# Optimization experiments

Measured on AMD Instinct MI355X. Metric: run time of the kernel, lower is better.

## Reference

```python
import jax, jax.numpy as jnp
import numpy as np

B, T, C, H = 4, 4096, 1024, 64

def setup_inputs() -> dict:
    key = jax.random.key(0)
    kx, kk, kq, kv = jax.random.split(key, 4)
    x = jax.random.normal(kx, (B, T, C), dtype=jnp.float32)
    Wk = jax.random.normal(kk, (C, H), dtype=jnp.float32) * (C ** -0.5)
    Wq = jax.random.normal(kq, (C, H), dtype=jnp.float32) * (C ** -0.5)
    Wv = jax.random.normal(kv, (C, H), dtype=jnp.float32) * (C ** -0.5)
    return {"x": x, "Wk": Wk, "Wq": Wq, "Wv": Wv}

def reference(x, Wk, Wq, Wv):
    Bb, Tt, Cc = x.shape
    k = jnp.einsum('btc,ch->bth', x, Wk)
    q = jnp.einsum('btc,ch->bth', x, Wq)
    v = jnp.einsum('btc,ch->bth', x, Wv)
    # NOTE: source scales by C**-0.5 with C = embed dim (not head_size)
    scores = jnp.einsum('bqh,bkh->bqk', q, k) * (Cc ** -0.5)
    causal = jnp.tril(jnp.ones((Tt, Tt), dtype=bool))
    scores = jnp.where(causal, scores, -jnp.inf)
    weights = jax.nn.softmax(scores, axis=-1)
    out = jnp.einsum('bqk,bkh->bqh', weights, v)
    return out
```

## Files before the change

kernel.cpp:

```cpp
#include <hip/hip_runtime.h>
#include <hip/hip_bf16.h>

typedef _Float16 f16x8 __attribute__((ext_vector_type(8)));
typedef _Float16 f16x4 __attribute__((ext_vector_type(4)));
typedef __fp16 fp16x2 __attribute__((ext_vector_type(2)));
typedef float f32x4 __attribute__((ext_vector_type(4)));

#define BATCH 4
#define SEQ 4096
#define EMB 1024
#define HEAD 64

__device__ __forceinline__ void async_copy16(const void* gsrc, void* ldst) {
  __builtin_amdgcn_global_load_lds(
      (const __attribute__((address_space(1))) void*)gsrc,
      (__attribute__((address_space(3))) void*)ldst,
      16, 0, 0);
}

__global__ __launch_bounds__(256) void wtrans_kernel(
    const float* __restrict__ Wk, const float* __restrict__ Wq,
    const float* __restrict__ Wv, _Float16* __restrict__ WT) {
  int id = blockIdx.x * 256 + threadIdx.x;
  int step = id / 1536;
  int rem = id - step * 1536;
  int G = rem / 192;
  int n = rem - G * 192;
  int sel = n >> 6;
  int col = n & 63;
  const float* src = (sel == 0) ? Wq : (sel == 1) ? Wk : Wv;
  const float scale = (sel == 0) ? 0.03125f : 1.0f;
  f16x8 u;
#pragma unroll
  for (int j = 0; j < 8; ++j) {
    int k = step * 64 + G * 8 + j;
    u[j] = (_Float16)(src[k * 64 + col] * scale);
  }
  *(f16x8*)(WT + (size_t)id * 8) = u;
}

__global__ __launch_bounds__(256) void proj_kernel(
    const float* __restrict__ x, const _Float16* __restrict__ WT,
    _Float16* __restrict__ Qh, _Float16* __restrict__ KT,
    _Float16* __restrict__ VT) {
  __shared__ _Float16 wtl[2][12288];
  __shared__ float xls[2][32 * 64];
  const int tid = threadIdx.x;
  const int wave = tid >> 6;
  const int lane = tid & 63;
  const int quad = lane >> 4;
  const int l16 = lane & 15;
  const int wm = wave & 1;
  const int wn = wave >> 1;
  const int rowblk = blockIdx.x * 32;

  const int lq = lane >> 4;
  const int pos = lane & 15;

  f32x4 acc[6];
#pragma unroll
  for (int t = 0; t < 6; ++t) acc[t] = (f32x4){0.f, 0.f, 0.f, 0.f};

#pragma unroll
  for (int i = 0; i < 6; ++i) {
    const int c = wave * 6 + i;
    async_copy16(WT + (size_t)c * 512 + lane * 8, (char*)&wtl[0][0] + c * 1024);
  }
#pragma unroll
  for (int i = 0; i < 2; ++i) {
    const int c = wave * 2 + i;
    const int rt = c * 4 + lq;
    const int u = pos ^ (rt & 7);
    async_copy16(x + (size_t)(rowblk + rt) * EMB + u * 4,
                 (char*)&xls[0][0] + c * 1024);
  }
  __syncthreads();

  const int rt = wm * 16 + l16;
  const int rb = rt & 7;
  const int ua = ((quad * 2) ^ rb) * 4;
  const int ub = ((quad * 2 + 1) ^ rb) * 4;
  const int uc = ((8 + quad * 2) ^ rb) * 4;
  const int ud = ((8 + quad * 2 + 1) ^ rb) * 4;

  int p = 0;
  for (int step = 0; step < 16; ++step) {
    if (step < 15) {
      const _Float16* wsrc = WT + (size_t)(step + 1) * 12288;
#pragma unroll
      for (int i = 0; i < 6; ++i) {
        const int c = wave * 6 + i;
        async_copy16(wsrc + (size_t)c * 512 + lane * 8,
                     (char*)&wtl[p ^ 1][0] + c * 1024);
      }
      const float* xsrc = x + (size_t)(step + 1) * 64;
#pragma unroll
      for (int i = 0; i < 2; ++i) {
        const int c = wave * 2 + i;
        const int rts = c * 4 + lq;
        const int u = pos ^ (rts & 7);
        async_copy16(xsrc + (size_t)(rowblk + rts) * EMB + u * 4,
                     (char*)&xls[p ^ 1][0] + c * 1024);
      }
    }
    const float* xl = &xls[p][rt * 64];
    const float4 xa = *(const float4*)(xl + ua);
    const float4 xb = *(const float4*)(xl + ub);
    const float4 xc = *(const float4*)(xl + uc);
    const float4 xd = *(const float4*)(xl + ud);
    fp16x2 p0 = __builtin_amdgcn_cvt_pkrtz(xa.x, xa.y);
    fp16x2 p1 = __builtin_amdgcn_cvt_pkrtz(xa.z, xa.w);
    fp16x2 p2 = __builtin_amdgcn_cvt_pkrtz(xb.x, xb.y);
    fp16x2 p3 = __builtin_amdgcn_cvt_pkrtz(xb.z, xb.w);
    f16x8 af0, af1;
    af0[0] = (_Float16)p0[0]; af0[1] = (_Float16)p0[1];
    af0[2] = (_Float16)p1[0]; af0[3] = (_Float16)p1[1];
    af0[4] = (_Float16)p2[0]; af0[5] = (_Float16)p2[1];
    af0[6] = (_Float16)p3[0]; af0[7] = (_Float16)p3[1];
    p0 = __builtin_amdgcn_cvt_pkrtz(xc.x, xc.y);
    p1 = __builtin_amdgcn_cvt_pkrtz(xc.z, xc.w);
    p2 = __builtin_amdgcn_cvt_pkrtz(xd.x, xd.y);
    p3 = __builtin_amdgcn_cvt_pkrtz(xd.z, xd.w);
    af1[0] = (_Float16)p0[0]; af1[1] = (_Float16)p0[1];
    af1[2] = (_Float16)p1[0]; af1[3] = (_Float16)p1[1];
    af1[4] = (_Float16)p2[0]; af1[5] = (_Float16)p2[1];
    af1[6] = (_Float16)p3[0]; af1[7] = (_Float16)p3[1];
#pragma unroll
    for (int t = 0; t < 6; ++t) {
      const int n = wn * 96 + t * 16 + l16;
      const f16x8 b0 = *(const f16x8*)&wtl[p][(size_t)((0 * 4 + quad) * 192 + n) * 8];
      const f16x8 b1 = *(const f16x8*)&wtl[p][(size_t)((1 * 4 + quad) * 192 + n) * 8];
      acc[t] = __builtin_amdgcn_mfma_f32_16x16x32_f16(af0, b0, acc[t], 0, 0, 0);
      acc[t] = __builtin_amdgcn_mfma_f32_16x16x32_f16(af1, b1, acc[t], 0, 0, 0);
    }
    __syncthreads();
    p ^= 1;
  }

  const int rowbase = rowblk + wm * 16;
  const int b = rowbase >> 12;
  const int trbase = (rowbase & 4095) + quad * 4;
#pragma unroll
  for (int t = 0; t < 6; ++t) {
    const int g = wn * 6 + t;
    if (g < 4) {
      const int h = g * 16 + l16;
#pragma unroll
      for (int r = 0; r < 4; ++r)
        Qh[(size_t)(rowbase + quad * 4 + r) * HEAD + h] = (_Float16)acc[t][r];
    } else if (g < 8) {
      const int h = (g - 4) * 16 + l16;
#pragma unroll
      for (int r = 0; r < 4; ++r) {
        const int t0 = trbase + r;
        const size_t ad = ((size_t)((b * 64 + (t0 >> 6)) * 8 + (h >> 3)) * 64 +
                           (t0 & 63)) * 8 + (h & 7);
        KT[ad] = (_Float16)acc[t][r];
      }
    } else {
      const int h = (g - 8) * 16 + l16;
      f16x4 pk;
      pk[0] = (_Float16)acc[t][0]; pk[1] = (_Float16)acc[t][1];
      pk[2] = (_Float16)acc[t][2]; pk[3] = (_Float16)acc[t][3];
      const size_t ad = ((size_t)((b * 64 + (trbase >> 6)) * 8 + ((trbase & 63) >> 3)) * 512) +
                        (size_t)h * 8 + (trbase & 7);
      *(f16x4*)(VT + ad) = pk;
    }
  }
}

__global__ __launch_bounds__(256) void flash_kernel(
    const _Float16* __restrict__ Qh, const _Float16* __restrict__ KT,
    const _Float16* __restrict__ VT, float* __restrict__ out) {
  __shared__ _Float16 myp[4][16 * 68];
  __shared__ float lds_o[2][16][68];
  __shared__ float lds_l[2][16];
  const int tid = threadIdx.x;
  const int w = tid >> 6;
  const int lane = tid & 63;
  const int quad = lane >> 4;
  const int l16 = lane & 15;
  const int b = blockIdx.x & 3;
  const int jj = blockIdx.x >> 2;
  const int t = w >> 1;
  const int kh = w & 1;
  const int j = t ? (255 - jj) : jj;
  const int qb = j * 16;
  const int nkt = (j >> 2) + 1;
  const int h1 = (nkt + 1) >> 1;
  const int lo = kh ? h1 : 0;
  const int hi = kh ? nkt : h1;

  const _Float16* Q = Qh + (size_t)b * SEQ * HEAD;
  const _Float16* KTb = KT + (size_t)b * 64 * 4096;
  const _Float16* VTb = VT + (size_t)b * 64 * 4096;
  const f32x4 zero = {0.f, 0.f, 0.f, 0.f};
  _Float16* mp = &myp[w][0];

  const f16x8 aq0 = *(const f16x8*)(Q + (size_t)(qb + l16) * HEAD + quad * 8);
  const f16x8 aq1 = *(const f16x8*)(Q + (size_t)(qb + l16) * HEAD + 32 + quad * 8);
  const int qrow = qb + quad * 4;

  f32x4 oc[4];
#pragma unroll
  for (int m = 0; m < 4; ++m) oc[m] = zero;
  float lacc[4] = {0.f, 0.f, 0.f, 0.f};

  f16x8 ka[4], kb[4];
  if (lo < hi) {
    const _Float16* kp = KTb + (size_t)lo * 4096;
#pragma unroll
    for (int s = 0; s < 4; ++s) {
      ka[s] = *(const f16x8*)(kp + (size_t)quad * 512 + (s * 16 + l16) * 8);
      kb[s] = *(const f16x8*)(kp + (size_t)(4 + quad) * 512 + (s * 16 + l16) * 8);
    }
  }

  for (int kt = lo; kt < hi; ++kt) {
    const _Float16* vp = VTb + (size_t)kt * 4096;
    f16x8 va[4], vb[4];
#pragma unroll
    for (int m = 0; m < 4; ++m) {
      va[m] = *(const f16x8*)(vp + (size_t)quad * 512 + (m * 16 + l16) * 8);
      vb[m] = *(const f16x8*)(vp + (size_t)(4 + quad) * 512 + (m * 16 + l16) * 8);
    }

    f32x4 sc[4];
#pragma unroll
    for (int s = 0; s < 4; ++s) {
      sc[s] = __builtin_amdgcn_mfma_f32_16x16x32_f16(aq0, ka[s], zero, 0, 0, 0);
      sc[s] = __builtin_amdgcn_mfma_f32_16x16x32_f16(aq1, kb[s], sc[s], 0, 0, 0);
    }

    if (kt + 1 < hi) {
      const _Float16* kp = KTb + (size_t)(kt + 1) * 4096;
#pragma unroll
      for (int s = 0; s < 4; ++s) {
        ka[s] = *(const f16x8*)(kp + (size_t)quad * 512 + (s * 16 + l16) * 8);
        kb[s] = *(const f16x8*)(kp + (size_t)(4 + quad) * 512 + (s * 16 + l16) * 8);
      }
    }

    const int kbase = kt * 64;
    if (kt == nkt - 1) {
#pragma unroll
      for (int s = 0; s < 4; ++s) {
#pragma unroll
        for (int r = 0; r < 4; ++r) {
          const float pv = (kbase + s * 16 + l16 > qrow + r) ? 0.f : __expf(sc[s][r]);
          lacc[r] += pv;
          mp[(quad * 4 + r) * 68 + s * 16 + l16] = (_Float16)pv;
        }
      }
    } else {
#pragma unroll
      for (int s = 0; s < 4; ++s) {
#pragma unroll
        for (int r = 0; r < 4; ++r) {
          const float pv = __expf(sc[s][r]);
          lacc[r] += pv;
          mp[(quad * 4 + r) * 68 + s * 16 + l16] = (_Float16)pv;
        }
      }
    }

    const f16x8 ap0 = *(const f16x8*)(mp + l16 * 68 + quad * 8);
    const f16x8 ap1 = *(const f16x8*)(mp + l16 * 68 + 32 + quad * 8);

#pragma unroll
    for (int m = 0; m < 4; ++m) {
      oc[m] = __builtin_amdgcn_mfma_f32_16x16x32_f16(ap0, va[m], oc[m], 0, 0, 0);
      oc[m] = __builtin_amdgcn_mfma_f32_16x16x32_f16(ap1, vb[m], oc[m], 0, 0, 0);
    }
  }

  float lr[4];
#pragma unroll
  for (int r = 0; r < 4; ++r) {
    float l = lacc[r];
    l += __shfl_xor(l, 1);
    l += __shfl_xor(l, 2);
    l += __shfl_xor(l, 4);
    l += __shfl_xor(l, 8);
    lr[r] = l;
  }

  if (kh) {
#pragma unroll
    for (int r = 0; r < 4; ++r) {
      if (l16 == 0) lds_l[t][quad * 4 + r] = lr[r];
#pragma unroll
      for (int m = 0; m < 4; ++m)
        lds_o[t][quad * 4 + r][m * 16 + l16] = oc[m][r];
    }
  }
  __syncthreads();
  if (!kh) {
#pragma unroll
    for (int r = 0; r < 4; ++r) {
      const float lsum = lr[r] + lds_l[t][quad * 4 + r];
      const float inv = 1.0f / lsum;
      float* op = out + ((size_t)b * SEQ + qb + quad * 4 + r) * HEAD + l16;
#pragma unroll
      for (int m = 0; m < 4; ++m)
        op[m * 16] = (oc[m][r] + lds_o[t][quad * 4 + r][m * 16 + l16]) * inv;
    }
  }
}

extern "C" void kernel_launch(void* const* d_in, const int* in_sizes, int n_in,
                              void* d_out, int out_size, void* d_ws, size_t ws_size,
                              hipStream_t stream) {
  const float* x  = (const float*)d_in[0];
  const float* Wk = (const float*)d_in[1];
  const float* Wq = (const float*)d_in[2];
  const float* Wv = (const float*)d_in[3];
  float* out = (float*)d_out;

  char* ws = (char*)d_ws;
  _Float16* Qh = (_Float16*)(ws);
  _Float16* KT = (_Float16*)(ws + (size_t)2 * 1024 * 1024);
  _Float16* VT = (_Float16*)(ws + (size_t)4 * 1024 * 1024);
  _Float16* WT = (_Float16*)(ws + (size_t)6 * 1024 * 1024);

  wtrans_kernel<<<96, 256, 0, stream>>>(Wk, Wq, Wv, WT);
  proj_kernel<<<512, 256, 0, stream>>>(x, WT, Qh, KT, VT);
  flash_kernel<<<512, 256, 0, stream>>>(Qh, KT, VT, out);
}
```

Before: 136.7 us.

## Triple-buffer x tiles in projection kernel with partial vmcnt waits

The projection kernel now keeps three LDS buffers for x tiles and prefetches two steps ahead, while weights stay double-buffered. It replaces the two __syncthreads per step with one explicit s_waitcnt vmcnt(2) plus s_barrier at the top of the loop, so the newest x prefetch can stay in flight. The aim is to hide global load latency for the fp32 x stream. This relies on hand-counted vmcnt values matching the per-thread async copy ordering, and it uses more LDS, which may lower occupancy.

Result: no change. 137.6 us (+0.7%).

```diff
diff --git a/kernel.cpp b/kernel.cpp
--- a/kernel.cpp
+++ b/kernel.cpp
@@ -44,7 +44,7 @@
     _Float16* __restrict__ Qh, _Float16* __restrict__ KT,
     _Float16* __restrict__ VT) {
   __shared__ _Float16 wtl[2][12288];
-  __shared__ float xls[2][32 * 64];
+  __shared__ float xls[3][32 * 64];
   const int tid = threadIdx.x;
   const int wave = tid >> 6;
   const int lane = tid & 63;
@@ -69,12 +69,19 @@
 #pragma unroll
   for (int i = 0; i < 2; ++i) {
     const int c = wave * 2 + i;
-    const int rt = c * 4 + lq;
-    const int u = pos ^ (rt & 7);
-    async_copy16(x + (size_t)(rowblk + rt) * EMB + u * 4,
+    const int rts = c * 4 + lq;
+    const int u = pos ^ (rts & 7);
+    async_copy16(x + (size_t)(rowblk + rts) * EMB + u * 4,
                  (char*)&xls[0][0] + c * 1024);
   }
-  __syncthreads();
+#pragma unroll
+  for (int i = 0; i < 2; ++i) {
+    const int c = wave * 2 + i;
+    const int rts = c * 4 + lq;
+    const int u = pos ^ (rts & 7);
+    async_copy16(x + (size_t)(rowblk + rts) * EMB + 64 + u * 4,
+                 (char*)&xls[1][0] + c * 1024);
+  }
 
   const int rt = wm * 16 + l16;
   const int rb = rt & 7;
@@ -83,27 +90,40 @@
   const int uc = ((8 + quad * 2) ^ rb) * 4;
   const int ud = ((8 + quad * 2 + 1) ^ rb) * 4;
 
-  int p = 0;
+  int pw = 0;
+  int x3 = 0;
+  int x3i = 2;
   for (int step = 0; step < 16; ++step) {
     if (step < 15) {
+      asm volatile("s_waitcnt vmcnt(2)" ::: "memory");
+    } else {
+      asm volatile("s_waitcnt vmcnt(0)" ::: "memory");
+    }
+    __builtin_amdgcn_sched_barrier(0);
+    __builtin_amdgcn_s_barrier();
+
+    if (step + 1 < 16) {
       const _Float16* wsrc = WT + (size_t)(step + 1) * 12288;
 #pragma unroll
       for (int i = 0; i < 6; ++i) {
         const int c = wave * 6 + i;
         async_copy16(wsrc + (size_t)c * 512 + lane * 8,
-                     (char*)&wtl[p ^ 1][0] + c * 1024);
-      }
-      const float* xsrc = x + (size_t)(step + 1) * 64;
+                     (char*)&wtl[pw ^ 1][0] + c * 1024);
+      }
+    }
+    if (step + 2 < 16) {
+      const float* xsrc = x + (size_t)(step + 2) * 64;
 #pragma unroll
       for (int i = 0; i < 2; ++i) {
         const int c = wave * 2 + i;
         const int rts = c * 4 + lq;
         const int u = pos ^ (rts & 7);
         async_copy16(xsrc + (size_t)(rowblk + rts) * EMB + u * 4,
-                     (char*)&xls[p ^ 1][0] + c * 1024);
-      }
-    }
-    const float* xl = &xls[p][rt * 64];
+                     (char*)&xls[x3i][0] + c * 1024);
+      }
+    }
+
+    const float* xl = &xls[x3][rt * 64];
     const float4 xa = *(const float4*)(xl + ua);
     const float4 xb = *(const float4*)(xl + ub);
     const float4 xc = *(const float4*)(xl + uc);
@@ -128,13 +148,14 @@
 #pragma unroll
     for (int t = 0; t < 6; ++t) {
       const int n = wn * 96 + t * 16 + l16;
-      const f16x8 b0 = *(const f16x8*)&wtl[p][(size_t)((0 * 4 + quad) * 192 + n) * 8];
-      const f16x8 b1 = *(const f16x8*)&wtl[p][(size_t)((1 * 4 + quad) * 192 + n) * 8];
+      const f16x8 b0 = *(const f16x8*)&wtl[pw][(size_t)((0 * 4 + quad) * 192 + n) * 8];
+      const f16x8 b1 = *(const f16x8*)&wtl[pw][(size_t)((1 * 4 + quad) * 192 + n) * 8];
       acc[t] = __builtin_amdgcn_mfma_f32_16x16x32_f16(af0, b0, acc[t], 0, 0, 0);
       acc[t] = __builtin_amdgcn_mfma_f32_16x16x32_f16(af1, b1, acc[t], 0, 0, 0);
     }
-    __syncthreads();
-    p ^= 1;
+    pw ^= 1;
+    x3 = (x3 == 2) ? 0 : x3 + 1;
+    x3i = (x3i == 2) ? 0 : x3i + 1;
   }
 
   const int rowbase = rowblk + wm * 16;
```
